# Optimization experiments

Hardware: AMD Instinct MI355X
Metric: run time of the kernel (lower is better)

Reference implementation:

```python
import jax, jax.numpy as jnp
import numpy as np

MARGIN = 1.0
NUM_CLASSES = 64

def setup_inputs() -> dict:
    key = jax.random.key(0)
    k1, k2 = jax.random.split(key)
    embeddings = jax.random.normal(k1, (4096, 512), dtype=jnp.float32)
    labels = jax.random.randint(k2, (4096,), 0, NUM_CLASSES, dtype=jnp.int64)
    return {"embeddings": embeddings, "labels": labels}

def _pairwise_dist(x):
    # Euclidean cdist via GEMM: ||xi||^2 + ||xj||^2 - 2 xi.xj, with a
    # grad-safe sqrt (zero distance -> zero, no nan gradient).
    sq_norms = jnp.sum(x * x, axis=1)                      # [B]
    sq = sq_norms[:, None] + sq_norms[None, :] - 2.0 * (x @ x.T)
    sq = jnp.maximum(sq, 0.0)
    pos = sq > 0.0
    return jnp.where(pos, jnp.sqrt(jnp.where(pos, sq, 1.0)), 0.0)

def reference(embeddings, labels):
    B = embeddings.shape[0]
    # L2 normalize (normalize=True)
    emb = embeddings / jnp.maximum(
        jnp.linalg.norm(embeddings, axis=1, keepdims=True), 1e-12)
    dist = _pairwise_dist(emb)                             # [B, B]
    same = labels[:, None] == labels[None, :]              # [B, B]
    eye = jnp.eye(B, dtype=bool)
    pos_mask = same & ~eye
    neg_mask = ~same
    pos_cnt = jnp.sum(pos_mask, axis=1)                    # [B]
    neg_cnt = jnp.sum(neg_mask, axis=1)
    # hard_positive=False -> mean over positive distances
    pos_stat = jnp.sum(jnp.where(pos_mask, dist, 0.0), axis=1) / jnp.maximum(pos_cnt, 1)
    # hardest negative = masked min (infinity trick)
    neg_stat = jnp.min(jnp.where(neg_mask, dist, jnp.inf), axis=1)
    per_row = jnp.maximum(pos_stat - neg_stat + MARGIN, 0.0)
    valid = (pos_cnt > 0) & (neg_cnt > 0)
    n_valid = jnp.sum(valid)
    total = jnp.sum(jnp.where(valid, per_row, 0.0))
    # reduction='mean' over valid rows; 0.0 if none valid
    return jnp.where(n_valid > 0, total / jnp.maximum(n_valid, 1), 0.0)
```

## Files before the change

kernel.cpp:

```cpp
#include <hip/hip_runtime.h>
#include <hip/hip_bf16.h>

#define BSZ 4096
#define DIM 512
#define NCLS 64
#define MARGIN_F 1.0f
#define NT 32
#define NPAIR (NT * (NT + 1) / 2)
#define NSL (2 * NT)
#define NFIN 16

typedef short short8 __attribute__((ext_vector_type(8)));
typedef float floatx4 __attribute__((ext_vector_type(4)));
typedef unsigned short u16;

#define OFF_PP  (BSZ * DIM * 2)
#define OFF_PN  (OFF_PP + NSL * BSZ * 4)
#define OFF_ACC (OFF_PN + NSL * BSZ * 4)

__device__ __forceinline__ u16 f2bf_rne(float f) {
    unsigned x = __float_as_uint(f);
    x += 0x7FFFu + ((x >> 16) & 1u);
    return (u16)(x >> 16);
}

__device__ __forceinline__ void gld_lds16(const u16* g, u16* l) {
    __builtin_amdgcn_global_load_lds(
        (const __attribute__((address_space(1))) unsigned int*)g,
        (__attribute__((address_space(3))) unsigned int*)l, 16, 0, 0);
}

__global__ __launch_bounds__(256) void ht_normalize(
        const float* __restrict__ emb, u16* __restrict__ ebf,
        float* __restrict__ acc_total, int* __restrict__ acc_nv,
        int* __restrict__ counter2) {
    const int lane = threadIdx.x & 63;
    const int row = blockIdx.x * 4 + (threadIdx.x >> 6);
    const float4* r4 = (const float4*)(emb + (size_t)row * DIM);
    float4 v0 = r4[lane * 2];
    float4 v1 = r4[lane * 2 + 1];
    float s = v0.x * v0.x + v0.y * v0.y + v0.z * v0.z + v0.w * v0.w
            + v1.x * v1.x + v1.y * v1.y + v1.z * v1.z + v1.w * v1.w;
#pragma unroll
    for (int off = 1; off < 64; off <<= 1) s += __shfl_xor(s, off);
    const float inv = 1.0f / fmaxf(sqrtf(s), 1e-12f);

    uint4 o;
    o.x = (unsigned)f2bf_rne(v0.x * inv) | ((unsigned)f2bf_rne(v0.y * inv) << 16);
    o.y = (unsigned)f2bf_rne(v0.z * inv) | ((unsigned)f2bf_rne(v0.w * inv) << 16);
    o.z = (unsigned)f2bf_rne(v1.x * inv) | ((unsigned)f2bf_rne(v1.y * inv) << 16);
    o.w = (unsigned)f2bf_rne(v1.z * inv) | ((unsigned)f2bf_rne(v1.w * inv) << 16);
    ((uint4*)(ebf + (size_t)row * DIM))[lane] = o;

    if (blockIdx.x == 0 && threadIdx.x == 0) {
        *acc_total = 0.0f; *acc_nv = 0; *counter2 = 0;
    }
}

__global__ __launch_bounds__(256) void ht_gemm_reduce(
        const u16* __restrict__ ebf, const int* __restrict__ labels,
        float* __restrict__ part_ps, unsigned* __restrict__ part_nm) {
    __shared__ u16 sA[2][128 * 32];
    __shared__ u16 sB[2][128 * 32];
    __shared__ int sLI[128];
    __shared__ int sLJ[128];

    int rem = blockIdx.x, by = 0;
    while (rem >= NT - by) { rem -= NT - by; ++by; }
    const int bx = by + rem;
    const bool offd = (bx != by);

    const int t = threadIdx.x;
    const int row0 = by * 128;
    const int col0 = bx * 128;

    if (t < 128) sLI[t] = labels[row0 + t];
    else         sLJ[t - 128] = labels[col0 + t - 128];

    const int lane = t & 63;
    const int wave = t >> 6;
    const int wr = (wave >> 1) * 64;
    const int wc = (wave & 1) * 64;
    const int l15 = lane & 15;
    const int quad = lane >> 4;

    const int s0 = t, s1 = 256 + t;
    const int gr0 = (s0 & 3) ^ ((s0 >> 3) & 3);
    const int gr1 = (s1 & 3) ^ ((s1 >> 3) & 3);
    const u16* gA0 = ebf + (size_t)(row0 + (s0 >> 2)) * DIM + gr0 * 8;
    const u16* gA1 = ebf + (size_t)(row0 + (s1 >> 2)) * DIM + gr1 * 8;
    const u16* gB0 = ebf + (size_t)(col0 + (s0 >> 2)) * DIM + gr0 * 8;
    const u16* gB1 = ebf + (size_t)(col0 + (s1 >> 2)) * DIM + gr1 * 8;
    const int lb0 = wave * 64 * 8;
    const int lb1 = (256 + wave * 64) * 8;

    const int qsw = (quad ^ ((l15 >> 1) & 3)) * 8;

    floatx4 acc[4][4] = {};

    gld_lds16(gA0, &sA[0][lb0]);
    gld_lds16(gA1, &sA[0][lb1]);
    gld_lds16(gB0, &sB[0][lb0]);
    gld_lds16(gB1, &sB[0][lb1]);

    int cur = 0;
    for (int ks = 0; ks < DIM / 32; ++ks) {
        __syncthreads();
        if (ks + 1 < DIM / 32) {
            const int kb = (ks + 1) * 32;
            gld_lds16(gA0 + kb, &sA[cur ^ 1][lb0]);
            gld_lds16(gA1 + kb, &sA[cur ^ 1][lb1]);
            gld_lds16(gB0 + kb, &sB[cur ^ 1][lb0]);
            gld_lds16(gB1 + kb, &sB[cur ^ 1][lb1]);
        }
        short8 af[4], bf[4];
#pragma unroll
        for (int mi = 0; mi < 4; ++mi)
            af[mi] = *(const short8*)(&sA[cur][(wr + mi * 16 + l15) * 32 + qsw]);
#pragma unroll
        for (int ni = 0; ni < 4; ++ni)
            bf[ni] = *(const short8*)(&sB[cur][(wc + ni * 16 + l15) * 32 + qsw]);
#pragma unroll
        for (int mi = 0; mi < 4; ++mi)
#pragma unroll
            for (int ni = 0; ni < 4; ++ni)
                acc[mi][ni] = __builtin_amdgcn_mfma_f32_16x16x32_bf16(
                    af[mi], bf[ni], acc[mi][ni], 0, 0, 0);
        cur ^= 1;
    }

    const float INF = __uint_as_float(0x7F800000u);
    const int rslice = 2 * bx + (wc >> 6);
    float psc[4] = {0.f, 0.f, 0.f, 0.f};
    float nmc[4] = {INF, INF, INF, INF};
#pragma unroll
    for (int mi = 0; mi < 4; ++mi) {
        const int rbase = wr + mi * 16 + quad * 4;
#pragma unroll
        for (int r = 0; r < 4; ++r) {
            const int rloc = rbase + r;
            const int gi = row0 + rloc;
            const int rl = sLI[rloc];
            float ps = 0.0f, nm = INF;
#pragma unroll
            for (int ni = 0; ni < 4; ++ni) {
                const int cloc = wc + ni * 16 + l15;
                const int gj = col0 + cloc;
                const int cl = sLJ[cloc];
                const float d = __builtin_amdgcn_sqrtf(
                    fmaxf(2.0f - 2.0f * acc[mi][ni][r], 0.0f));
                if (rl == cl) {
                    if (gi != gj) ps += d;
                    if (offd) psc[ni] += d;
                } else {
                    nm = fminf(nm, d);
                    if (offd) nmc[ni] = fminf(nmc[ni], d);
                }
            }
#pragma unroll
            for (int off = 1; off < 16; off <<= 1) {
                ps += __shfl_xor(ps, off);
                nm = fminf(nm, __shfl_xor(nm, off));
            }
            if (l15 == 0) {
                part_ps[rslice * BSZ + gi] = ps;
                part_nm[rslice * BSZ + gi] = __float_as_uint(nm);
            }
        }
    }
    if (offd) {
        const int cslice = 2 * by + (wr >> 6);
#pragma unroll
        for (int ni = 0; ni < 4; ++ni) {
            float ps = psc[ni], nm = nmc[ni];
            ps += __shfl_xor(ps, 16); ps += __shfl_xor(ps, 32);
            nm = fminf(nm, __shfl_xor(nm, 16));
            nm = fminf(nm, __shfl_xor(nm, 32));
            if (quad == 0) {
                const int gj = col0 + wc + ni * 16 + l15;
                part_ps[cslice * BSZ + gj] = ps;
                part_nm[cslice * BSZ + gj] = __float_as_uint(nm);
            }
        }
    }
}

__global__ __launch_bounds__(256) void ht_finalize(
        const float* __restrict__ part_ps, const unsigned* __restrict__ part_nm,
        const int* __restrict__ labels, float* __restrict__ acc_total,
        int* __restrict__ acc_nv, int* __restrict__ counter2,
        float* __restrict__ out) {
    __shared__ int hist[NCLS];
    __shared__ float sT[4];
    __shared__ int sN[4];
    const int t = threadIdx.x;
    if (t < NCLS) hist[t] = 0;
    __syncthreads();
    for (int i = t; i < BSZ; i += 256) atomicAdd(&hist[labels[i]], 1);
    __syncthreads();

    const int j = blockIdx.x * 256 + t;
    float ps = 0.0f;
    float nm = __uint_as_float(0x7F800000u);
#pragma unroll 8
    for (int s = 0; s < NSL; ++s) {
        ps += part_ps[s * BSZ + j];
        nm = fminf(nm, __uint_as_float(part_nm[s * BSZ + j]));
    }
    const int cnt = hist[labels[j]];
    const int pc = cnt - 1;
    const int nc = BSZ - cnt;
    float loss = 0.0f;
    int lv = 0;
    if (pc > 0 && nc > 0) {
        loss = fmaxf(ps / (float)pc - nm + MARGIN_F, 0.0f);
        lv = 1;
    }
#pragma unroll
    for (int off = 1; off < 64; off <<= 1) {
        loss += __shfl_xor(loss, off);
        lv += __shfl_xor(lv, off);
    }
    if ((t & 63) == 0) { sT[t >> 6] = loss; sN[t >> 6] = lv; }
    __syncthreads();
    if (t == 0) {
        const float tt = sT[0] + sT[1] + sT[2] + sT[3];
        const int nn = sN[0] + sN[1] + sN[2] + sN[3];
        __hip_atomic_fetch_add(acc_total, tt, __ATOMIC_ACQ_REL,
                               __HIP_MEMORY_SCOPE_AGENT);
        __hip_atomic_fetch_add(acc_nv, nn, __ATOMIC_ACQ_REL,
                               __HIP_MEMORY_SCOPE_AGENT);
        const int old2 = __hip_atomic_fetch_add(counter2, 1, __ATOMIC_ACQ_REL,
                                                __HIP_MEMORY_SCOPE_AGENT);
        if (old2 == NFIN - 1) {
            const float ft = __hip_atomic_load(acc_total, __ATOMIC_ACQUIRE,
                                               __HIP_MEMORY_SCOPE_AGENT);
            const int fn = __hip_atomic_load(acc_nv, __ATOMIC_ACQUIRE,
                                             __HIP_MEMORY_SCOPE_AGENT);
            out[0] = (fn > 0) ? ft / (float)fn : 0.0f;
        }
    }
}

extern "C" void kernel_launch(void* const* d_in, const int* in_sizes, int n_in,
                              void* d_out, int out_size, void* d_ws, size_t ws_size,
                              hipStream_t stream) {
    const float* emb = (const float*)d_in[0];
    const int* labels = (const int*)d_in[1];
    float* out = (float*)d_out;
    char* ws = (char*)d_ws;

    u16* ebf = (u16*)ws;
    float* part_ps = (float*)(ws + OFF_PP);
    unsigned* part_nm = (unsigned*)(ws + OFF_PN);
    float* acc_total = (float*)(ws + OFF_ACC);
    int* acc_nv = (int*)(ws + OFF_ACC + 4);
    int* counter2 = (int*)(ws + OFF_ACC + 8);

    ht_normalize<<<BSZ / 4, 256, 0, stream>>>(emb, ebf, acc_total, acc_nv,
                                              counter2);
    ht_gemm_reduce<<<NPAIR, 256, 0, stream>>>(ebf, labels, part_ps, part_nm);
    ht_finalize<<<NFIN, 256, 0, stream>>>(part_ps, part_nm, labels,
                                          acc_total, acc_nv, counter2, out);
}
```

Before: 95.77 us.

## Split each 128x128 GEMM tile into two 64-row blocks to double the grid

Each upper-triangular tile pair now runs as two blocks, each covering 64 rows against 128 columns, so the grid doubles from 528 to 1056 blocks and per-thread accumulators drop from 16 to 8 fragments. Column-side partial sums and minima are combined between the two row-halves of waves through shared memory before being written, which keeps the slice layout compatible with finalize. The aim is better occupancy and fuller use of the MI355X CUs. The cost is that each block reloads the B tile, so B traffic doubles, and the epilogue gains an extra barrier.

Measured after the change: 93.56 us. 1.02x faster.

```diff
diff --git a/kernel.cpp b/kernel.cpp
--- a/kernel.cpp
+++ b/kernel.cpp
@@ -7,6 +7,7 @@
 #define MARGIN_F 1.0f
 #define NT 32
 #define NPAIR (NT * (NT + 1) / 2)
+#define NBLK (NPAIR * 2)
 #define NSL (2 * NT)
 #define NFIN 16
 
@@ -60,68 +61,72 @@
 __global__ __launch_bounds__(256) void ht_gemm_reduce(
         const u16* __restrict__ ebf, const int* __restrict__ labels,
         float* __restrict__ part_ps, unsigned* __restrict__ part_nm) {
-    __shared__ u16 sA[2][128 * 32];
+    __shared__ u16 sA[2][64 * 32];
     __shared__ u16 sB[2][128 * 32];
-    __shared__ int sLI[128];
+    __shared__ int sLI[64];
     __shared__ int sLJ[128];
-
-    int rem = blockIdx.x, by = 0;
+    __shared__ float sCPps[128];
+    __shared__ float sCPnm[128];
+
+    const int p = blockIdx.x >> 1;
+    const int h = blockIdx.x & 1;
+    int rem = p, by = 0;
     while (rem >= NT - by) { rem -= NT - by; ++by; }
     const int bx = by + rem;
     const bool offd = (bx != by);
 
     const int t = threadIdx.x;
-    const int row0 = by * 128;
+    const int row0 = by * 128 + h * 64;
     const int col0 = bx * 128;
 
-    if (t < 128) sLI[t] = labels[row0 + t];
-    else         sLJ[t - 128] = labels[col0 + t - 128];
+    if (t < 64) sLI[t] = labels[row0 + t];
+    else if (t < 192) sLJ[t - 64] = labels[col0 + (t - 64)];
 
     const int lane = t & 63;
     const int wave = t >> 6;
-    const int wr = (wave >> 1) * 64;
+    const int wr = (wave >> 1) * 32;
     const int wc = (wave & 1) * 64;
     const int l15 = lane & 15;
     const int quad = lane >> 4;
 
-    const int s0 = t, s1 = 256 + t;
-    const int gr0 = (s0 & 3) ^ ((s0 >> 3) & 3);
-    const int gr1 = (s1 & 3) ^ ((s1 >> 3) & 3);
-    const u16* gA0 = ebf + (size_t)(row0 + (s0 >> 2)) * DIM + gr0 * 8;
-    const u16* gA1 = ebf + (size_t)(row0 + (s1 >> 2)) * DIM + gr1 * 8;
-    const u16* gB0 = ebf + (size_t)(col0 + (s0 >> 2)) * DIM + gr0 * 8;
-    const u16* gB1 = ebf + (size_t)(col0 + (s1 >> 2)) * DIM + gr1 * 8;
-    const int lb0 = wave * 64 * 8;
-    const int lb1 = (256 + wave * 64) * 8;
+    const int sa = t;
+    const int ga = (sa & 3) ^ ((sa >> 3) & 3);
+    const u16* gA0 = ebf + (size_t)(row0 + (sa >> 2)) * DIM + ga * 8;
+    const int sb0 = t, sb1 = 256 + t;
+    const int gb0 = (sb0 & 3) ^ ((sb0 >> 3) & 3);
+    const int gb1 = (sb1 & 3) ^ ((sb1 >> 3) & 3);
+    const u16* gB0 = ebf + (size_t)(col0 + (sb0 >> 2)) * DIM + gb0 * 8;
+    const u16* gB1 = ebf + (size_t)(col0 + (sb1 >> 2)) * DIM + gb1 * 8;
+    const int lbA = wave * 64 * 8;
+    const int lbB0 = wave * 64 * 8;
+    const int lbB1 = (256 + wave * 64) * 8;
 
     const int qsw = (quad ^ ((l15 >> 1) & 3)) * 8;
 
-    floatx4 acc[4][4] = {};
-
-    gld_lds16(gA0, &sA[0][lb0]);
-    gld_lds16(gA1, &sA[0][lb1]);
-    gld_lds16(gB0, &sB[0][lb0]);
-    gld_lds16(gB1, &sB[0][lb1]);
+    floatx4 acc[2][4] = {};
+
+    gld_lds16(gA0, &sA[0][lbA]);
+    gld_lds16(gB0, &sB[0][lbB0]);
+    gld_lds16(gB1, &sB[0][lbB1]);
 
     int cur = 0;
     for (int ks = 0; ks < DIM / 32; ++ks) {
         __syncthreads();
         if (ks + 1 < DIM / 32) {
             const int kb = (ks + 1) * 32;
-            gld_lds16(gA0 + kb, &sA[cur ^ 1][lb0]);
-            gld_lds16(gA1 + kb, &sA[cur ^ 1][lb1]);
-            gld_lds16(gB0 + kb, &sB[cur ^ 1][lb0]);
-            gld_lds16(gB1 + kb, &sB[cur ^ 1][lb1]);
-        }
-        short8 af[4], bf[4];
-#pragma unroll
-        for (int mi = 0; mi < 4; ++mi)
+            gld_lds16(gA0 + kb, &sA[cur ^ 1][lbA]);
+            gld_lds16(gB0 + kb, &sB[cur ^ 1][lbB0]);
+            gld_lds16(gB1 + kb, &sB[cur ^ 1][lbB1]);
+        }
+        short8 af[2], bf[4];
+#pragma unroll
+        for (int mi = 0; mi < 2; ++mi)
             af[mi] = *(const short8*)(&sA[cur][(wr + mi * 16 + l15) * 32 + qsw]);
 #pragma unroll
         for (int ni = 0; ni < 4; ++ni)
             bf[ni] = *(const short8*)(&sB[cur][(wc + ni * 16 + l15) * 32 + qsw]);
 #pragma unroll
-        for (int mi = 0; mi < 4; ++mi)
+        for (int mi = 0; mi < 2; ++mi)
 #pragma unroll
             for (int ni = 0; ni < 4; ++ni)
                 acc[mi][ni] = __builtin_amdgcn_mfma_f32_16x16x32_bf16(
@@ -134,7 +139,7 @@
     float psc[4] = {0.f, 0.f, 0.f, 0.f};
     float nmc[4] = {INF, INF, INF, INF};
 #pragma unroll
-    for (int mi = 0; mi < 4; ++mi) {
+    for (int mi = 0; mi < 2; ++mi) {
         const int rbase = wr + mi * 16 + quad * 4;
 #pragma unroll
         for (int r = 0; r < 4; ++r) {
@@ -169,15 +174,32 @@
         }
     }
     if (offd) {
-        const int cslice = 2 * by + (wr >> 6);
+        const int cslice = 2 * by + h;
+        float cps[4], cnm[4];
 #pragma unroll
         for (int ni = 0; ni < 4; ++ni) {
             float ps = psc[ni], nm = nmc[ni];
             ps += __shfl_xor(ps, 16); ps += __shfl_xor(ps, 32);
             nm = fminf(nm, __shfl_xor(nm, 16));
             nm = fminf(nm, __shfl_xor(nm, 32));
-            if (quad == 0) {
-                const int gj = col0 + wc + ni * 16 + l15;
+            cps[ni] = ps; cnm[ni] = nm;
+        }
+        if (wave >= 2 && quad == 0) {
+#pragma unroll
+            for (int ni = 0; ni < 4; ++ni) {
+                const int cl = wc + ni * 16 + l15;
+                sCPps[cl] = cps[ni];
+                sCPnm[cl] = cnm[ni];
+            }
+        }
+        __syncthreads();
+        if (wave < 2 && quad == 0) {
+#pragma unroll
+            for (int ni = 0; ni < 4; ++ni) {
+                const int cl = wc + ni * 16 + l15;
+                const int gj = col0 + cl;
+                const float ps = cps[ni] + sCPps[cl];
+                const float nm = fminf(cnm[ni], sCPnm[cl]);
                 part_ps[cslice * BSZ + gj] = ps;
                 part_nm[cslice * BSZ + gj] = __float_as_uint(nm);
             }
@@ -259,7 +281,7 @@
 
     ht_normalize<<<BSZ / 4, 256, 0, stream>>>(emb, ebf, acc_total, acc_nv,
                                               counter2);
-    ht_gemm_reduce<<<NPAIR, 256, 0, stream>>>(ebf, labels, part_ps, part_nm);
+    ht_gemm_reduce<<<NBLK, 256, 0, stream>>>(ebf, labels, part_ps, part_nm);
     ht_finalize<<<NFIN, 256, 0, stream>>>(part_ps, part_nm, labels,
                                           acc_total, acc_nv, counter2, out);
 }
```
